# Kernel optimization log

Hardware: AMD Instinct MI355X
Metric: run time of the kernel (lower is better)

## Reference

```python
import jax, jax.numpy as jnp
import numpy as np

LN_EPS = 1e-5
NORM_EPS = 1e-12
TEMPERATURE = 0.5


def _project(h, W1, b1, W2, b2, g, beta):
    # projection head: Linear -> ReLU -> Linear -> LayerNorm, then L2 normalize
    x = jnp.maximum(h @ W1 + b1, 0.0) @ W2 + b2          # [B, P]
    mu = jnp.mean(x, axis=-1, keepdims=True)
    var = jnp.mean(jnp.square(x - mu), axis=-1, keepdims=True)
    x = (x - mu) * jax.lax.rsqrt(var + LN_EPS) * g + beta
    n = jnp.linalg.norm(x, axis=-1, keepdims=True)
    return x / jnp.maximum(n, NORM_EPS)                   # [B, P]


def setup_inputs() -> dict:
    key = jax.random.key(0)
    ks = jax.random.split(key, 8)
    B, H, P, K, NBUF = 16384, 2048, 256, 64, 2000
    Hh = H // 2
    return {
        "hidden_states": jax.random.normal(ks[0], (B, H), jnp.float32),
        "positive_hidden": jax.random.normal(ks[1], (B, H), jnp.float32),
        "neg_buffer": jax.random.normal(ks[2], (NBUF, P), jnp.float32),
        "W1": jax.random.normal(ks[3], (H, Hh), jnp.float32) * (1.0 / np.sqrt(H)),
        "b1": jnp.zeros((Hh,), jnp.float32),
        "W2": jax.random.normal(ks[4], (Hh, P), jnp.float32) * (1.0 / np.sqrt(Hh)),
        "b2": jnp.zeros((P,), jnp.float32),
        "ln_gamma": jnp.ones((P,), jnp.float32),
        "ln_beta": jnp.zeros((P,), jnp.float32),
        "neg_indices": jax.random.randint(ks[5], (B, K), 0, NBUF, jnp.int32),
    }


def reference(hidden_states, positive_hidden, neg_buffer, W1, b1, W2, b2,
              ln_gamma, ln_beta, neg_indices):
    anchors = _project(hidden_states, W1, b1, W2, b2, ln_gamma, ln_beta)      # [B,P]
    positives = _project(positive_hidden, W1, b1, W2, b2, ln_gamma, ln_beta)  # [B,P]
    # negatives are detached in the original (buffer stores .detach() features)
    negs = jax.lax.stop_gradient(neg_buffer)[neg_indices]                      # [B,K,P]
    pos_sim = jnp.einsum('bp,bp->b', anchors, positives) / TEMPERATURE        # [B]
    neg_sims = jnp.einsum('bkp,bp->bk', negs, anchors) / TEMPERATURE          # [B,K]
    logits = jnp.concatenate([pos_sim[:, None], neg_sims], axis=1)            # [B,1+K]
    # cross-entropy with label 0 for every anchor, averaged over the batch
    loss = -jnp.mean(jax.nn.log_softmax(logits, axis=-1)[:, 0])
    return loss
```

## Files before the change

### kernel.cpp

```cpp
#include <hip/hip_runtime.h>
#include <hip/hip_bf16.h>
#include <cstdint>

#define BATCH   16384
#define HDIM    2048
#define HHDIM   1024
#define PDIM    256
#define KNEG    64
#define NBUF    2000
#define M1      (2 * BATCH)

typedef float  f32x4  __attribute__((ext_vector_type(4)));
typedef __bf16 bf16x8 __attribute__((ext_vector_type(8)));

typedef __attribute__((address_space(3))) unsigned int       lds_u32;
typedef __attribute__((address_space(1))) const unsigned int glb_u32;

__device__ __forceinline__ void gload_lds16(const void* g, void* l) {
  __builtin_amdgcn_global_load_lds((glb_u32*)g, (lds_u32*)l, 16, 0, 0);
}

__device__ __forceinline__ float dot4(f32x4 a, f32x4 b) {
  return a[0]*b[0] + a[1]*b[1] + a[2]*b[2] + a[3]*b[3];
}

#define VMCNT(n) asm volatile("s_waitcnt vmcnt(" #n ")" ::: "memory")
#define LGKM(n)  asm volatile("s_waitcnt lgkmcnt(" #n ")" ::: "memory")

__global__ void transpose_cast_kernel(const float* __restrict__ src,
                                      __bf16* __restrict__ dst, int K, int N) {
  __shared__ float tile[32][33];
  int bn = blockIdx.x * 32, bk = blockIdx.y * 32;
  int tx = threadIdx.x, ty = threadIdx.y;
  for (int j = 0; j < 32; j += 8)
    tile[ty + j][tx] = src[(size_t)(bk + ty + j) * N + bn + tx];
  __syncthreads();
  for (int j = 0; j < 32; j += 8)
    dst[(size_t)(bn + ty + j) * K + bk + tx] = (__bf16)tile[tx][ty + j];
}

template <int KD, int BMH, int NBt, bool AF32, bool RELU_OUT, bool LNFUSE, int GRID>
__global__ __launch_bounds__(512)
void gemm_8ph(const void* __restrict__ A0v, const void* __restrict__ A1v,
              const __bf16* __restrict__ Bt, const float* __restrict__ bias,
              const float* __restrict__ lng, const float* __restrict__ lnb,
              void* __restrict__ Cv) {
  static_assert(!LNFUSE || NBt == 1, "LN fusion needs full rows per block");
  constexpr int KT    = KD / 64;
  constexpr int MI    = BMH / 32;
  constexpr int AHALF = BMH * 64;
  constexpr int BHALF = 128 * 64;
  constexpr int ASTEP = 2 * AHALF;
  constexpr int BSTEP = 2 * BHALF;
  constexpr int NDIM  = NBt * 256;
  constexpr int AUL   = BMH / 64;

  __shared__ __bf16 lA[2 * ASTEP];
  __shared__ __bf16 lB[2 * BSTEP];

  constexpr int Q = GRID / 8;
  int bid = blockIdx.x;
  int swb = (bid & 7) * Q + (bid >> 3);
  const int mb = swb / NBt, nb = swb % NBt;
  const long mrow0 = (long)mb * (2 * BMH);
  const int  ncol0 = nb * 256;

  const int tid = threadIdx.x;
  const int wid = tid >> 6, lane = tid & 63;
  const int wr = wid >> 2, wc = wid & 3;
  const int fl = lane & 15, fh = lane >> 4;

  int aoff[MI][2], boff[2][2];
  #pragma unroll
  for (int mi = 0; mi < MI; ++mi)
    #pragma unroll
    for (int ks = 0; ks < 2; ++ks) {
      int row = wr * (BMH / 2) + mi * 16 + fl;
      aoff[mi][ks] = row * 64 + (((ks * 4 + fh) ^ (row & 7)) * 8);
    }
  #pragma unroll
  for (int ni = 0; ni < 2; ++ni)
    #pragma unroll
    for (int ks = 0; ks < 2; ++ks) {
      int row = wc * 32 + ni * 16 + fl;
      boff[ni][ks] = row * 64 + (((ks * 4 + fh) ^ (row & 7)) * 8);
    }

  const int r0 = tid >> 3, sl = tid & 7;
  long bS[2][2];
  #pragma unroll
  for (int h = 0; h < 2; ++h)
    #pragma unroll
    for (int i = 0; i < 2; ++i) {
      int rr = r0 + i * 64;
      int ss = sl ^ (rr & 7);
      bS[h][i] = ((long)(ncol0 + h * 128 + rr)) * KD + ss * 8;
    }
  const int dstw = wid * 512;

  auto stB = [&](int h, int t) {
    __bf16* base = lB + (t & 1) * BSTEP + h * BHALF + dstw;
    #pragma unroll
    for (int i = 0; i < 2; ++i)
      gload_lds16(Bt + bS[h][i] + (long)t * 64, (void*)(base + i * 4096));
  };

  long aS[2][AUL];
  const float* Afp = nullptr;
  if constexpr (AF32) {
    const float* A0 = (const float*)A0v;
    const float* A1 = (const float*)A1v;
    Afp = (mrow0 < BATCH) ? (A0 + (size_t)mrow0 * KD)
                          : (A1 + (size_t)(mrow0 - BATCH) * KD);
  } else {
    #pragma unroll
    for (int h = 0; h < 2; ++h)
      #pragma unroll
      for (int i = 0; i < AUL; ++i) {
        int rr = r0 + i * 64;
        int ss = sl ^ (rr & 7);
        aS[h][i] = (mrow0 + h * BMH + rr) * (long)KD + ss * 8;
      }
  }

  auto stA = [&](int h, int t) {
    __bf16* base = lA + (t & 1) * ASTEP + h * AHALF + dstw;
    #pragma unroll
    for (int i = 0; i < AUL; ++i)
      gload_lds16((const __bf16*)A0v + aS[h][i] + (long)t * 64,
                  (void*)(base + i * 4096));
  };

  const int rowA = tid >> 2, pA = tid & 3;
  f32x4 aq[4];
  auto issueA = [&](int h, int t) {
    const float* p = Afp + (size_t)(h * 128 + rowA) * KD + t * 64 + pA * 16;
    aq[0] = *(const f32x4*)(p);
    aq[1] = *(const f32x4*)(p + 4);
    aq[2] = *(const f32x4*)(p + 8);
    aq[3] = *(const f32x4*)(p + 12);
  };
  auto writeA = [&](int h, int t) {
    bf16x8 w0, w1;
    #pragma unroll
    for (int j = 0; j < 4; ++j) {
      w0[j] = (__bf16)aq[0][j]; w0[4 + j] = (__bf16)aq[1][j];
      w1[j] = (__bf16)aq[2][j]; w1[4 + j] = (__bf16)aq[3][j];
    }
    __bf16* base = lA + (t & 1) * ASTEP + h * AHALF + rowA * 64;
    *(bf16x8*)(base + (((2 * pA)     ^ (rowA & 7)) * 8)) = w0;
    *(bf16x8*)(base + (((2 * pA + 1) ^ (rowA & 7)) * 8)) = w1;
  };

  bf16x8 areg[MI][2], breg0[2][2], breg1[2][2];
  auto loadA = [&](int mh, int s) {
    const __bf16* base = lA + (s & 1) * ASTEP + mh * AHALF;
    #pragma unroll
    for (int mi = 0; mi < MI; ++mi)
      #pragma unroll
      for (int ks = 0; ks < 2; ++ks)
        areg[mi][ks] = *(const bf16x8*)(base + aoff[mi][ks]);
  };
  auto loadB = [&](bf16x8 (&br)[2][2], int nh, int s) {
    const __bf16* base = lB + (s & 1) * BSTEP + nh * BHALF;
    #pragma unroll
    for (int ni = 0; ni < 2; ++ni)
      #pragma unroll
      for (int ks = 0; ks < 2; ++ks)
        br[ni][ks] = *(const bf16x8*)(base + boff[ni][ks]);
  };

  f32x4 acc[2][2][MI][2] = {};

#define PHASE_MFMA(mh, nh, BR)                                                \
  __builtin_amdgcn_s_setprio(1);                                              \
  _Pragma("unroll")                                                           \
  for (int ks = 0; ks < 2; ++ks) {                                            \
    _Pragma("unroll")                                                         \
    for (int mi = 0; mi < MI; ++mi) {                                         \
      _Pragma("unroll")                                                       \
      for (int ni = 0; ni < 2; ++ni)                                          \
        acc[mh][nh][mi][ni] = __builtin_amdgcn_mfma_f32_16x16x32_bf16(        \
            areg[mi][ks], BR[ni][ks], acc[mh][nh][mi][ni], 0, 0, 0);          \
    }                                                                         \
  }                                                                           \
  __builtin_amdgcn_s_setprio(0);

  if constexpr (AF32) {
    issueA(0, 0); writeA(0, 0);
    issueA(1, 0); writeA(1, 0);
    issueA(0, 1); writeA(0, 1);
    issueA(1, 1); writeA(1, 1);
  } else {
    stA(0, 0); stA(1, 0); stA(0, 1); stA(1, 1);
  }
  stB(0, 0); stB(1, 0); stB(0, 1); stB(1, 1);
  if constexpr (AF32)           { VMCNT(4); LGKM(0); }
  else if constexpr (BMH == 128){ VMCNT(8); }
  else                          { VMCNT(6); }
  __builtin_amdgcn_s_barrier();
  __builtin_amdgcn_sched_barrier(0);

  for (int s = 0; s < KT; ++s) {
    loadA(0, s);
    loadB(breg0, 0, s);
    if constexpr (AF32) { if (s >= 1 && s + 1 < KT) issueA(1, s + 1); }
    if (s >= 1 && s + 1 < KT) stB(0, s + 1);
    if constexpr (BMH == 128) LGKM(8);
    __builtin_amdgcn_s_barrier();
    LGKM(0);
    __builtin_amdgcn_sched_barrier(0);
    PHASE_MFMA(0, 0, breg0);
    __builtin_amdgcn_s_barrier();

    loadB(breg1, 1, s);
    if constexpr (AF32) { if (s >= 1 && s + 1 < KT) writeA(1, s + 1); }
    else                { if (s >= 1 && s + 1 < KT) stA(1, s + 1); }
    __builtin_amdgcn_s_barrier();
    LGKM(0);
    __builtin_amdgcn_sched_barrier(0);
    PHASE_MFMA(0, 1, breg1);
    __builtin_amdgcn_s_barrier();

    loadA(1, s);
    if constexpr (AF32) { if (s + 2 < KT) issueA(0, s + 2); }
    else                { if (s + 2 < KT) stA(0, s + 2); }
    __builtin_amdgcn_s_barrier();
    LGKM(0);
    __builtin_amdgcn_sched_barrier(0);
    PHASE_MFMA(1, 1, breg1);
    __builtin_amdgcn_s_barrier();

    if constexpr (AF32) { if (s + 2 < KT) writeA(0, s + 2); }
    if (s + 2 < KT) stB(1, s + 2);
    __builtin_amdgcn_s_barrier();
    LGKM(0);
    __builtin_amdgcn_sched_barrier(0);
    PHASE_MFMA(1, 0, breg0);
    if (s + 2 < KT) {
      if constexpr (AF32)            { VMCNT(2); }
      else if constexpr (BMH == 128) { VMCNT(4); }
      else                           { VMCNT(3); }
    } else {
      VMCNT(0);
    }
    __builtin_amdgcn_s_barrier();
    __builtin_amdgcn_sched_barrier(0);
  }

#undef PHASE_MFMA

  if constexpr (LNFUSE) {
    float (*s1p)[4] = (float(*)[4])((float*)lA);
    float (*s2p)[4] = (float(*)[4])((float*)lA + 512);
    float (*n2p)[4] = (float(*)[4])((float*)lA + 1024);

    float v[2][2][MI][2][4];
    float gg[2][2], bb[2][2];
    #pragma unroll
    for (int nh = 0; nh < 2; ++nh)
      #pragma unroll
      for (int ni = 0; ni < 2; ++ni) {
        int c = nh * 128 + wc * 32 + ni * 16 + fl;
        float bv = bias[c];
        gg[nh][ni] = lng[c]; bb[nh][ni] = lnb[c];
        #pragma unroll
        for (int mh = 0; mh < 2; ++mh)
          #pragma unroll
          for (int mi = 0; mi < MI; ++mi)
            #pragma unroll
            for (int r = 0; r < 4; ++r)
              v[mh][nh][mi][ni][r] = acc[mh][nh][mi][ni][r] + bv;
      }

    #pragma unroll
    for (int mh = 0; mh < 2; ++mh)
      #pragma unroll
      for (int mi = 0; mi < MI; ++mi)
        #pragma unroll
        for (int r = 0; r < 4; ++r) {
          float s1 = 0.0f, s2 = 0.0f;
          #pragma unroll
          for (int nh = 0; nh < 2; ++nh)
            #pragma unroll
            for (int ni = 0; ni < 2; ++ni) {
              float x = v[mh][nh][mi][ni][r];
              s1 += x; s2 += x * x;
            }
          for (int m = 1; m < 16; m <<= 1) {
            s1 += __shfl_xor(s1, m, 64);
            s2 += __shfl_xor(s2, m, 64);
          }
          if (fl == 0) {
            int lr = mh * 64 + wr * 32 + mi * 16 + fh * 4 + r;
            s1p[lr][wc] = s1; s2p[lr][wc] = s2;
          }
        }
    __syncthreads();

    float n2loc[2][MI][4];
    #pragma unroll
    for (int mh = 0; mh < 2; ++mh)
      #pragma unroll
      for (int mi = 0; mi < MI; ++mi)
        #pragma unroll
        for (int r = 0; r < 4; ++r) {
          int lr = mh * 64 + wr * 32 + mi * 16 + fh * 4 + r;
          float t1 = s1p[lr][0] + s1p[lr][1] + s1p[lr][2] + s1p[lr][3];
          float t2 = s2p[lr][0] + s2p[lr][1] + s2p[lr][2] + s2p[lr][3];
          float mu = t1 * (1.0f / PDIM);
          float var = t2 * (1.0f / PDIM) - mu * mu;
          float rstd = rsqrtf(var + 1e-5f);
          float n2 = 0.0f;
          #pragma unroll
          for (int nh = 0; nh < 2; ++nh)
            #pragma unroll
            for (int ni = 0; ni < 2; ++ni) {
              float y = (v[mh][nh][mi][ni][r] - mu) * rstd * gg[nh][ni] + bb[nh][ni];
              v[mh][nh][mi][ni][r] = y;
              n2 += y * y;
            }
          for (int m = 1; m < 16; m <<= 1) n2 += __shfl_xor(n2, m, 64);
          n2loc[mh][mi][r] = n2;
        }
    #pragma unroll
    for (int mh = 0; mh < 2; ++mh)
      #pragma unroll
      for (int mi = 0; mi < MI; ++mi)
        #pragma unroll
        for (int r = 0; r < 4; ++r)
          if (fl == 0) {
            int lr = mh * 64 + wr * 32 + mi * 16 + fh * 4 + r;
            n2p[lr][wc] = n2loc[mh][mi][r];
          }
    __syncthreads();

    #pragma unroll
    for (int mh = 0; mh < 2; ++mh)
      #pragma unroll
      for (int mi = 0; mi < MI; ++mi)
        #pragma unroll
        for (int r = 0; r < 4; ++r) {
          int lr = mh * 64 + wr * 32 + mi * 16 + fh * 4 + r;
          float t = n2p[lr][0] + n2p[lr][1] + n2p[lr][2] + n2p[lr][3];
          float sc = 1.0f / fmaxf(sqrtf(t), 1e-12f);
          #pragma unroll
          for (int nh = 0; nh < 2; ++nh)
            #pragma unroll
            for (int ni = 0; ni < 2; ++ni) {
              int c = nh * 128 + wc * 32 + ni * 16 + fl;
              ((float*)Cv)[(mrow0 + lr) * NDIM + c] = v[mh][nh][mi][ni][r] * sc;
            }
        }
  } else {
    #pragma unroll
    for (int mh = 0; mh < 2; ++mh)
      #pragma unroll
      for (int nh = 0; nh < 2; ++nh)
        #pragma unroll
        for (int ni = 0; ni < 2; ++ni) {
          int col = ncol0 + nh * 128 + wc * 32 + ni * 16 + fl;
          float bv = bias[col];
          #pragma unroll
          for (int mi = 0; mi < MI; ++mi)
            #pragma unroll
            for (int r = 0; r < 4; ++r) {
              long row = mrow0 + mh * BMH + wr * (BMH / 2) + mi * 16 + fh * 4 + r;
              float x = acc[mh][nh][mi][ni][r] + bv;
              if constexpr (RELU_OUT) {
                x = fmaxf(x, 0.0f);
                ((__bf16*)Cv)[row * NDIM + col] = (__bf16)x;
              } else {
                ((float*)Cv)[row * NDIM + col] = x;
              }
            }
        }
  }
}

__global__ __launch_bounds__(256)
void loss_kernel(const float* __restrict__ X, const float* __restrict__ negbuf,
                 const int* __restrict__ nidx, float* __restrict__ partials) {
  __shared__ float lsum[4];
  int b    = blockIdx.x * 4 + (threadIdx.x >> 6);
  int lane = threadIdx.x & 63;
  int g = lane >> 4, lg = lane & 15;

  const float* arow = X + (size_t)b * PDIM;
  const float* prow = X + (size_t)(BATCH + b) * PDIM;

  f32x4 a4[4];
  for (int j = 0; j < 4; ++j) a4[j] = *(const f32x4*)(arow + lg * 16 + j * 4);

  float ps = 0.0f;
  for (int j = 0; j < 4; ++j) {
    f32x4 p = *(const f32x4*)(prow + lg * 16 + j * 4);
    ps += dot4(a4[j], p);
  }
  for (int m = 1; m < 16; m <<= 1) ps += __shfl_xor(ps, m, 64);
  float pos = ps * 2.0f;

  float myneg = -3.0e38f;
  for (int k4 = 0; k4 < 16; ++k4) {
    int k = k4 * 4 + g;
    int idx = nidx[(size_t)b * KNEG + k];
    const float* nrow = negbuf + (size_t)idx * PDIM;
    float sv = 0.0f;
    for (int j = 0; j < 4; ++j) {
      f32x4 nv = *(const f32x4*)(nrow + lg * 16 + j * 4);
      sv += dot4(a4[j], nv);
    }
    for (int m = 1; m < 16; m <<= 1) sv += __shfl_xor(sv, m, 64);
    if (lg == k4) myneg = sv * 2.0f;
  }

  float mx = myneg;
  for (int m = 1; m < 64; m <<= 1) mx = fmaxf(mx, __shfl_xor(mx, m, 64));
  mx = fmaxf(mx, pos);
  float e = expf(myneg - mx);
  for (int m = 1; m < 64; m <<= 1) e += __shfl_xor(e, m, 64);
  float tot = e + expf(pos - mx);
  float lb = -(pos - mx - logf(tot));

  if (lane == 0) lsum[threadIdx.x >> 6] = lb;
  __syncthreads();
  if (threadIdx.x == 0)
    partials[blockIdx.x] = lsum[0] + lsum[1] + lsum[2] + lsum[3];
}

__global__ void finalize_kernel(const float* __restrict__ partials,
                                float* __restrict__ out) {
  __shared__ float ls[4];
  int tid = threadIdx.x;
  float s = 0.0f;
  for (int i = tid; i < 4096; i += 256) s += partials[i];
  for (int m = 1; m < 64; m <<= 1) s += __shfl_xor(s, m, 64);
  if ((tid & 63) == 0) ls[tid >> 6] = s;
  __syncthreads();
  if (tid == 0) out[0] = (ls[0] + ls[1] + ls[2] + ls[3]) * (1.0f / BATCH);
}

extern "C" void kernel_launch(void* const* d_in, const int* in_sizes, int n_in,
                              void* d_out, int out_size, void* d_ws, size_t ws_size,
                              hipStream_t stream) {
  const float* hidden   = (const float*)d_in[0];
  const float* positive = (const float*)d_in[1];
  const float* negbuf   = (const float*)d_in[2];
  const float* W1       = (const float*)d_in[3];
  const float* b1       = (const float*)d_in[4];
  const float* W2       = (const float*)d_in[5];
  const float* b2       = (const float*)d_in[6];
  const float* gamma    = (const float*)d_in[7];
  const float* beta     = (const float*)d_in[8];
  const int*   nidx     = (const int*)d_in[9];
  float* out = (float*)d_out;

  char* ws = (char*)d_ws;
  __bf16* W1T      = (__bf16*)(ws);
  __bf16* W2T      = (__bf16*)(ws + 4194304);
  __bf16* Y1       = (__bf16*)(ws + 4718592);
  float*  X        = (float*) (ws + 71827456);
  float*  partials = (float*) (ws + 105381888);

  transpose_cast_kernel<<<dim3(HHDIM / 32, HDIM / 32), dim3(32, 8), 0, stream>>>(
      W1, W1T, HDIM, HHDIM);
  transpose_cast_kernel<<<dim3(PDIM / 32, HHDIM / 32), dim3(32, 8), 0, stream>>>(
      W2, W2T, HHDIM, PDIM);

  gemm_8ph<HDIM, 128, HHDIM / 256, true, true, false, (M1 / 256) * (HHDIM / 256)>
      <<<(M1 / 256) * (HHDIM / 256), 512, 0, stream>>>(
          hidden, positive, W1T, b1, nullptr, nullptr, Y1);

  gemm_8ph<HHDIM, 64, PDIM / 256, false, false, true, (M1 / 128) * (PDIM / 256)>
      <<<(M1 / 128) * (PDIM / 256), 512, 0, stream>>>(
          Y1, nullptr, W2T, b2, gamma, beta, X);

  loss_kernel<<<BATCH / 4, 256, 0, stream>>>(X, negbuf, nidx, partials);
  finalize_kernel<<<1, 256, 0, stream>>>(partials, out);
}
```

Measured before the change: 334.4 us.

## Pre-cast GEMM1 activations and negative buffer to bf16 in separate kernels

Adds standalone cast kernels that convert hidden/positive activations and the negative buffer to bf16 ahead of time. GEMM1 can then use the same async global-to-LDS bf16 loading path as GEMM2, replacing the in-loop fp32 register load, convert and LDS write. The loss kernel reads bf16 negatives, halving gather bytes. The cost is an extra full read and write pass over the 256 MB of fp32 activations, plus reduced precision on negatives.

```diff
diff --git a/kernel.cpp b/kernel.cpp
--- a/kernel.cpp
+++ b/kernel.cpp
@@ -26,6 +26,20 @@
 
 #define VMCNT(n) asm volatile("s_waitcnt vmcnt(" #n ")" ::: "memory")
 #define LGKM(n)  asm volatile("s_waitcnt lgkmcnt(" #n ")" ::: "memory")
+
+__global__ __launch_bounds__(256)
+void cast_bf16_kernel(const float* __restrict__ src, __bf16* __restrict__ dst,
+                      long n8) {
+  long i = (long)blockIdx.x * blockDim.x + threadIdx.x;
+  long stride = (long)gridDim.x * blockDim.x;
+  for (; i < n8; i += stride) {
+    f32x4 a = ((const f32x4*)src)[2 * i];
+    f32x4 b = ((const f32x4*)src)[2 * i + 1];
+    bf16x8 w;
+    for (int j = 0; j < 4; ++j) { w[j] = (__bf16)a[j]; w[4 + j] = (__bf16)b[j]; }
+    ((bf16x8*)dst)[i] = w;
+  }
+}
 
 __global__ void transpose_cast_kernel(const float* __restrict__ src,
                                       __bf16* __restrict__ dst, int K, int N) {
@@ -39,10 +53,10 @@
     dst[(size_t)(bn + ty + j) * K + bk + tx] = (__bf16)tile[tx][ty + j];
 }
 
-template <int KD, int BMH, int NBt, bool AF32, bool RELU_OUT, bool LNFUSE, int GRID>
+template <int KD, int BMH, int NBt, bool RELU_OUT, bool LNFUSE, int GRID>
 __global__ __launch_bounds__(512)
-void gemm_8ph(const void* __restrict__ A0v, const void* __restrict__ A1v,
-              const __bf16* __restrict__ Bt, const float* __restrict__ bias,
+void gemm_8ph(const __bf16* __restrict__ A, const __bf16* __restrict__ Bt,
+              const float* __restrict__ bias,
               const float* __restrict__ lng, const float* __restrict__ lnb,
               void* __restrict__ Cv) {
   static_assert(!LNFUSE || NBt == 1, "LN fusion needs full rows per block");
@@ -87,69 +101,35 @@
     }
 
   const int r0 = tid >> 3, sl = tid & 7;
-  long bS[2][2];
+  long aS[2][AUL], bS[2][2];
   #pragma unroll
-  for (int h = 0; h < 2; ++h)
+  for (int h = 0; h < 2; ++h) {
+    #pragma unroll
+    for (int i = 0; i < AUL; ++i) {
+      int rr = r0 + i * 64;
+      int ss = sl ^ (rr & 7);
+      aS[h][i] = (mrow0 + h * BMH + rr) * (long)KD + ss * 8;
+    }
     #pragma unroll
     for (int i = 0; i < 2; ++i) {
       int rr = r0 + i * 64;
       int ss = sl ^ (rr & 7);
       bS[h][i] = ((long)(ncol0 + h * 128 + rr)) * KD + ss * 8;
     }
+  }
   const int dstw = wid * 512;
 
+  auto stA = [&](int h, int t) {
+    __bf16* base = lA + (t & 1) * ASTEP + h * AHALF + dstw;
+    #pragma unroll
+    for (int i = 0; i < AUL; ++i)
+      gload_lds16(A + aS[h][i] + (long)t * 64, (void*)(base + i * 4096));
+  };
   auto stB = [&](int h, int t) {
     __bf16* base = lB + (t & 1) * BSTEP + h * BHALF + dstw;
     #pragma unroll
     for (int i = 0; i < 2; ++i)
       gload_lds16(Bt + bS[h][i] + (long)t * 64, (void*)(base + i * 4096));
-  };
-
-  long aS[2][AUL];
-  const float* Afp = nullptr;
-  if constexpr (AF32) {
-    const float* A0 = (const float*)A0v;
-    const float* A1 = (const float*)A1v;
-    Afp = (mrow0 < BATCH) ? (A0 + (size_t)mrow0 * KD)
-                          : (A1 + (size_t)(mrow0 - BATCH) * KD);
-  } else {
-    #pragma unroll
-    for (int h = 0; h < 2; ++h)
-      #pragma unroll
-      for (int i = 0; i < AUL; ++i) {
-        int rr = r0 + i * 64;
-        int ss = sl ^ (rr & 7);
-        aS[h][i] = (mrow0 + h * BMH + rr) * (long)KD + ss * 8;
-      }
-  }
-
-  auto stA = [&](int h, int t) {
-    __bf16* base = lA + (t & 1) * ASTEP + h * AHALF + dstw;
-    #pragma unroll
-    for (int i = 0; i < AUL; ++i)
-      gload_lds16((const __bf16*)A0v + aS[h][i] + (long)t * 64,
-                  (void*)(base + i * 4096));
-  };
-
-  const int rowA = tid >> 2, pA = tid & 3;
-  f32x4 aq[4];
-  auto issueA = [&](int h, int t) {
-    const float* p = Afp + (size_t)(h * 128 + rowA) * KD + t * 64 + pA * 16;
-    aq[0] = *(const f32x4*)(p);
-    aq[1] = *(const f32x4*)(p + 4);
-    aq[2] = *(const f32x4*)(p + 8);
-    aq[3] = *(const f32x4*)(p + 12);
-  };
-  auto writeA = [&](int h, int t) {
-    bf16x8 w0, w1;
-    #pragma unroll
-    for (int j = 0; j < 4; ++j) {
-      w0[j] = (__bf16)aq[0][j]; w0[4 + j] = (__bf16)aq[1][j];
-      w1[j] = (__bf16)aq[2][j]; w1[4 + j] = (__bf16)aq[3][j];
-    }
-    __bf16* base = lA + (t & 1) * ASTEP + h * AHALF + rowA * 64;
-    *(bf16x8*)(base + (((2 * pA)     ^ (rowA & 7)) * 8)) = w0;
-    *(bf16x8*)(base + (((2 * pA + 1) ^ (rowA & 7)) * 8)) = w1;
   };
 
   bf16x8 areg[MI][2], breg0[2][2], breg1[2][2];
@@ -186,25 +166,15 @@
   }                                                                           \
   __builtin_amdgcn_s_setprio(0);
 
-  if constexpr (AF32) {
-    issueA(0, 0); writeA(0, 0);
-    issueA(1, 0); writeA(1, 0);
-    issueA(0, 1); writeA(0, 1);
-    issueA(1, 1); writeA(1, 1);
-  } else {
-    stA(0, 0); stA(1, 0); stA(0, 1); stA(1, 1);
-  }
-  stB(0, 0); stB(1, 0); stB(0, 1); stB(1, 1);
-  if constexpr (AF32)           { VMCNT(4); LGKM(0); }
-  else if constexpr (BMH == 128){ VMCNT(8); }
-  else                          { VMCNT(6); }
+  stA(0, 0); stB(0, 0); stA(1, 0); stB(1, 0);
+  stA(0, 1); stB(1, 1); stB(0, 1); stA(1, 1);
+  if constexpr (BMH == 128) { VMCNT(8); } else { VMCNT(6); }
   __builtin_amdgcn_s_barrier();
   __builtin_amdgcn_sched_barrier(0);
 
   for (int s = 0; s < KT; ++s) {
     loadA(0, s);
     loadB(breg0, 0, s);
-    if constexpr (AF32) { if (s >= 1 && s + 1 < KT) issueA(1, s + 1); }
     if (s >= 1 && s + 1 < KT) stB(0, s + 1);
     if constexpr (BMH == 128) LGKM(8);
     __builtin_amdgcn_s_barrier();
@@ -214,8 +184,7 @@
     __builtin_amdgcn_s_barrier();
 
     loadB(breg1, 1, s);
-    if constexpr (AF32) { if (s >= 1 && s + 1 < KT) writeA(1, s + 1); }
-    else                { if (s >= 1 && s + 1 < KT) stA(1, s + 1); }
+    if (s >= 1 && s + 1 < KT) stA(1, s + 1);
     __builtin_amdgcn_s_barrier();
     LGKM(0);
     __builtin_amdgcn_sched_barrier(0);
@@ -223,24 +192,19 @@
     __builtin_amdgcn_s_barrier();
 
     loadA(1, s);
-    if constexpr (AF32) { if (s + 2 < KT) issueA(0, s + 2); }
-    else                { if (s + 2 < KT) stA(0, s + 2); }
+    if (s + 2 < KT) stA(0, s + 2);
     __builtin_amdgcn_s_barrier();
     LGKM(0);
     __builtin_amdgcn_sched_barrier(0);
     PHASE_MFMA(1, 1, breg1);
     __builtin_amdgcn_s_barrier();
 
-    if constexpr (AF32) { if (s + 2 < KT) writeA(0, s + 2); }
     if (s + 2 < KT) stB(1, s + 2);
     __builtin_amdgcn_s_barrier();
-    LGKM(0);
     __builtin_amdgcn_sched_barrier(0);
     PHASE_MFMA(1, 0, breg0);
     if (s + 2 < KT) {
-      if constexpr (AF32)            { VMCNT(2); }
-      else if constexpr (BMH == 128) { VMCNT(4); }
-      else                           { VMCNT(3); }
+      if constexpr (BMH == 128) { VMCNT(4); } else { VMCNT(3); }
     } else {
       VMCNT(0);
     }
@@ -379,7 +343,7 @@
 }
 
 __global__ __launch_bounds__(256)
-void loss_kernel(const float* __restrict__ X, const float* __restrict__ negbuf,
+void loss_kernel(const float* __restrict__ X, const __bf16* __restrict__ negb,
                  const int* __restrict__ nidx, float* __restrict__ partials) {
   __shared__ float lsum[4];
   int b    = blockIdx.x * 4 + (threadIdx.x >> 6);
@@ -389,13 +353,20 @@
   const float* arow = X + (size_t)b * PDIM;
   const float* prow = X + (size_t)(BATCH + b) * PDIM;
 
-  f32x4 a4[4];
-  for (int j = 0; j < 4; ++j) a4[j] = *(const f32x4*)(arow + lg * 16 + j * 4);
+  float a16[16];
+  #pragma unroll
+  for (int j = 0; j < 4; ++j) {
+    f32x4 av = *(const f32x4*)(arow + lg * 16 + j * 4);
+    #pragma unroll
+    for (int e = 0; e < 4; ++e) a16[j * 4 + e] = av[e];
+  }
 
   float ps = 0.0f;
+  #pragma unroll
   for (int j = 0; j < 4; ++j) {
     f32x4 p = *(const f32x4*)(prow + lg * 16 + j * 4);
-    ps += dot4(a4[j], p);
+    #pragma unroll
+    for (int e = 0; e < 4; ++e) ps += a16[j * 4 + e] * p[e];
   }
   for (int m = 1; m < 16; m <<= 1) ps += __shfl_xor(ps, m, 64);
   float pos = ps * 2.0f;
@@ -404,11 +375,13 @@
   for (int k4 = 0; k4 < 16; ++k4) {
     int k = k4 * 4 + g;
     int idx = nidx[(size_t)b * KNEG + k];
-    const float* nrow = negbuf + (size_t)idx * PDIM;
+    const __bf16* nrow = negb + (size_t)idx * PDIM;
     float sv = 0.0f;
-    for (int j = 0; j < 4; ++j) {
-      f32x4 nv = *(const f32x4*)(nrow + lg * 16 + j * 4);
-      sv += dot4(a4[j], nv);
+    #pragma unroll
+    for (int j = 0; j < 2; ++j) {
+      bf16x8 nv = *(const bf16x8*)(nrow + lg * 16 + j * 8);
+      #pragma unroll
+      for (int e = 0; e < 8; ++e) sv += a16[j * 8 + e] * (float)nv[e];
     }
     for (int m = 1; m < 16; m <<= 1) sv += __shfl_xor(sv, m, 64);
     if (lg == k4) myneg = sv * 2.0f;
@@ -456,25 +429,38 @@
   float* out = (float*)d_out;
 
   char* ws = (char*)d_ws;
-  __bf16* W1T      = (__bf16*)(ws);
-  __bf16* W2T      = (__bf16*)(ws + 4194304);
-  __bf16* Y1       = (__bf16*)(ws + 4718592);
-  float*  X        = (float*) (ws + 71827456);
-  float*  partials = (float*) (ws + 105381888);
+  const size_t OFF_Y1   = 134217728;
+  const size_t OFF_W1T  = OFF_Y1 + 67108864;
+  const size_t OFF_W2T  = OFF_W1T + 4194304;
+  const size_t OFF_NEGB = OFF_W2T + 524288;
+  const size_t OFF_PART = OFF_NEGB + 1048576;
+
+  __bf16* Abf      = (__bf16*)(ws);
+  __bf16* Y1       = (__bf16*)(ws + OFF_Y1);
+  __bf16* W1T      = (__bf16*)(ws + OFF_W1T);
+  __bf16* W2T      = (__bf16*)(ws + OFF_W2T);
+  __bf16* negb     = (__bf16*)(ws + OFF_NEGB);
+  float*  partials = (float*) (ws + OFF_PART);
+  float*  X        = (float*) (ws);
 
   transpose_cast_kernel<<<dim3(HHDIM / 32, HDIM / 32), dim3(32, 8), 0, stream>>>(
       W1, W1T, HDIM, HHDIM);
   transpose_cast_kernel<<<dim3(PDIM / 32, HHDIM / 32), dim3(32, 8), 0, stream>>>(
       W2, W2T, HHDIM, PDIM);
 
-  gemm_8ph<HDIM, 128, HHDIM / 256, true, true, false, (M1 / 256) * (HHDIM / 256)>
+  const long n8 = (long)BATCH * HDIM / 8;
+  cast_bf16_kernel<<<2048, 256, 0, stream>>>(hidden, Abf, n8);
+  cast_bf16_kernel<<<2048, 256, 0, stream>>>(positive, Abf + (size_t)BATCH * HDIM, n8);
+  cast_bf16_kernel<<<256, 256, 0, stream>>>(negbuf, negb, (long)NBUF * PDIM / 8);
+
+  gemm_8ph<HDIM, 128, HHDIM / 256, true, false, (M1 / 256) * (HHDIM / 256)>
       <<<(M1 / 256) * (HHDIM / 256), 512, 0, stream>>>(
-          hidden, positive, W1T, b1, nullptr, nullptr, Y1);
-
-  gemm_8ph<HHDIM, 64, PDIM / 256, false, false, true, (M1 / 128) * (PDIM / 256)>
+          Abf, W1T, b1, nullptr, nullptr, Y1);
+
+  gemm_8ph<HHDIM, 64, PDIM / 256, false, true, (M1 / 128) * (PDIM / 256)>
       <<<(M1 / 128) * (PDIM / 256), 512, 0, stream>>>(
-          Y1, nullptr, W2T, b2, gamma, beta, X);
-
-  loss_kernel<<<BATCH / 4, 256, 0, stream>>>(X, negbuf, nidx, partials);
+          Y1, W2T, b2, gamma, beta, X);
+
+  loss_kernel<<<BATCH / 4, 256, 0, stream>>>(X, negb, nidx, partials);
   finalize_kernel<<<1, 256, 0, stream>>>(partials, out);
 }
```

Measured after the change: 303.2 us. -9.3%, faster.
